# Kernel tuning notes

Hardware: AMD Instinct MI355X
Metric: run time of the kernel (lower is better)

Reference implementation:

```python
import jax, jax.numpy as jnp
import numpy as np
from jax import lax

ALPHA = 2.0       # spikingjelly ATan surrogate default alpha
NUM_HEADS = 8
V_TH = 1.0

@jax.custom_vjp
def spike(x):
    return (x >= 0.0).astype(x.dtype)

def _spike_fwd(x):
    return spike(x), x

def _spike_bwd(x, g):
    # ATan surrogate: alpha/2 / (1 + (pi/2 * alpha * x)^2)
    return (g * (ALPHA / 2.0) / (1.0 + (jnp.pi / 2.0 * ALPHA * x) ** 2),)

spike.defvjp(_spike_fwd, _spike_bwd)

def lif(x, w):
    # ParametricLIFNode, step_mode='m', decay_input=True, hard reset to 0,
    # detach_reset=True. x: [T, ...]; w: learned scalar, decay = sigmoid(w).
    decay = jax.nn.sigmoid(w)
    def step(v, xt):
        v = v + (xt - v) * decay
        s = spike(v - V_TH)
        v = v * (1.0 - lax.stop_gradient(s))  # detach_reset hard reset
        return v, s
    _, s = lax.scan(step, jnp.zeros_like(x[0]), x)
    return s

def layernorm(x, g, b, eps=1e-5):
    m = x.mean(-1, keepdims=True)
    var = ((x - m) ** 2).mean(-1, keepdims=True)
    return (x - m) / jnp.sqrt(var + eps) * g + b

def setup_inputs() -> dict:
    key = jax.random.key(0)
    ks = jax.random.split(key, 16)
    T, B, C, H, W = 4, 16, 512, 16, 16
    hidden = 4 * C
    s = 0.02
    inp = {
        'x': jax.random.normal(ks[0], (T, B, C, H, W), jnp.float32),
        'conv_w': jax.random.normal(ks[1], (C, 1, 3, 3), jnp.float32) * s,
        'conv_b': jnp.zeros((C,), jnp.float32),
        'ln1_g': jnp.ones((C,), jnp.float32),
        'ln1_b': jnp.zeros((C,), jnp.float32),
        'qkv_w': jax.random.normal(ks[2], (3 * C, C), jnp.float32) * s,
        'proj_w': jax.random.normal(ks[3], (C, C), jnp.float32) * s,
        'proj_b': jnp.zeros((C,), jnp.float32),
        'ln2_g': jnp.ones((C,), jnp.float32),
        'ln2_b': jnp.zeros((C,), jnp.float32),
        'fc1_w': jax.random.normal(ks[4], (hidden, C), jnp.float32) * s,
        'fc1_b': jnp.zeros((hidden,), jnp.float32),
        'fc2_w': jax.random.normal(ks[5], (C, hidden), jnp.float32) * s,
        'fc2_b': jnp.zeros((C,), jnp.float32),
        'lif_w': jnp.zeros((8,), jnp.float32),  # init_tau=2 -> w=0
    }
    return inp

def reference(x, conv_w, conv_b, ln1_g, ln1_b, qkv_w, proj_w, proj_b,
              ln2_g, ln2_b, fc1_w, fc1_b, fc2_w, fc2_b, lif_w):
    T, B, C, H, W = x.shape
    N = H * W
    nH = NUM_HEADS
    d = C // nH
    scale = d ** -0.5

    # conv positional embedding on spikes, residual
    s = lif(x, lif_w[0])
    sf = s.reshape(T * B, C, H, W)
    pos = lax.conv_general_dilated(
        sf, conv_w, (1, 1), 'SAME', feature_group_count=C,
        dimension_numbers=('NCHW', 'OIHW', 'NCHW'))
    pos = pos + conv_b[None, :, None, None]
    x = x + pos.reshape(T, B, C, H, W)

    # tokens: [T, B, N, C]
    xt = x.reshape(T, B, C, N).transpose(0, 1, 3, 2)

    # spiking linear attention
    h = lif(layernorm(xt, ln1_g, ln1_b), lif_w[1])
    qkv = h @ qkv_w.T                              # [T,B,N,3C]
    qkv = qkv.reshape(T, B, N, 3, nH, d).transpose(3, 0, 1, 4, 2, 5)  # [3,T,B,h,N,d]
    q = lif(qkv[0], lif_w[2])
    k = lif(qkv[1], lif_w[3])
    v = lif(qkv[2], lif_w[4])
    kv = jnp.einsum('tbhnd,tbhne->tbhde', k, v)    # [T,B,h,d,d]
    a = jnp.einsum('tbhnd,tbhde->tbhne', q, kv) * scale
    a = a.transpose(0, 1, 3, 2, 4).reshape(T, B, N, C)
    a = lif(a, lif_w[5])
    a = a @ proj_w.T + proj_b
    xt = xt + a

    # spiking MLP
    h = lif(layernorm(xt, ln2_g, ln2_b), lif_w[6])
    h = h @ fc1_w.T + fc1_b
    h = lif(h, lif_w[7])
    h = h @ fc2_w.T + fc2_b
    xt = xt + h

    return xt.transpose(0, 1, 3, 2).reshape(T, B, C, H, W)
```

## Files before the change

### kernel.cpp

```cpp
#include <hip/hip_runtime.h>

typedef unsigned long long u64;
typedef unsigned int u32;
typedef float  floatx4 __attribute__((ext_vector_type(4)));
typedef short  short8  __attribute__((ext_vector_type(8)));

#define T_ 4

static __device__ __forceinline__ float b2f(unsigned short u){
  union { unsigned int i; float f; } x; x.i = ((unsigned int)u) << 16; return x.f;
}
static __device__ __forceinline__ unsigned short f2b(float f){
  unsigned int u = __float_as_uint(f);
  unsigned int r = (u + 0x7FFFu + ((u >> 16) & 1u)) >> 16;
  return (unsigned short)r;
}
static __device__ __forceinline__ float sigmoidf_(float x){ return 1.f / (1.f + expf(-x)); }

static __device__ __forceinline__ void gll16(const void* g, void* l){
  __builtin_amdgcn_global_load_lds(
      (const __attribute__((address_space(1))) void*)g,
      (__attribute__((address_space(3))) void*)l, 16, 0, 0);
}

__global__ __launch_bounds__(256) void wsplit_kernel(const float* __restrict__ qkvw,
    const float* __restrict__ projw, const float* __restrict__ fc1w,
    const float* __restrict__ fc2w, unsigned short* __restrict__ hi,
    unsigned short* __restrict__ lo){
  int i = blockIdx.x * 256 + threadIdx.x;
  const float* src; int off;
  if (i < 786432)      { src = qkvw; off = i; }
  else if (i < 1048576){ src = projw; off = i - 786432; }
  else if (i < 2097152){ src = fc1w;  off = i - 1048576; }
  else                 { src = fc2w;  off = i - 2097152; }
  float f = src[off];
  unsigned short h = f2b(f);
  float r = f - b2f(h);
  hi[i] = h; lo[i] = f2b(r);
}

__global__ __launch_bounds__(256) void conv_lif_kernel(const float* __restrict__ x,
    const float* __restrict__ cw, const float* __restrict__ cb,
    const float* __restrict__ lifw, float* __restrict__ xt){
  __shared__ __align__(16) float xs[16 * 260];
  __shared__ u64 sbits[16][5];
  int bb = blockIdx.x & 15, cg = blockIdx.x >> 4;
  int c0 = cg * 16;
  int tid = threadIdx.x;
  int lane = tid & 63, w = tid >> 6;
  int cl = tid & 15;
  float D = sigmoidf_(lifw[0]);
  float cwv[9];
  #pragma unroll
  for (int j = 0; j < 9; ++j) cwv[j] = cw[(c0 + cl) * 9 + j];
  float cbv = cb[c0 + cl];
  float v[16];
  #pragma unroll
  for (int k = 0; k < 16; ++k) v[k] = 0.f;

  for (int t = 0; t < T_; ++t){
    #pragma unroll
    for (int j = 0; j < 4; ++j){
      int kk = __builtin_amdgcn_readfirstlane(w + 4 * j);
      const float* grow = x + (((size_t)t * 16 + bb) * 512 + c0 + kk) * 256 + lane * 4;
      gll16(grow, &xs[kk * 260]);
    }
    __syncthreads();
    #pragma unroll
    for (int k = 0; k < 16; ++k){
      float xv = xs[k * 260 + tid];
      v[k] = v[k] + (xv - v[k]) * D;
      bool sp = v[k] >= 1.f;
      u64 bal = __ballot(sp);
      if (lane == 0) sbits[k][w] = bal;
      v[k] = sp ? 0.f : v[k];
    }
    __syncthreads();
    u64 sw0 = sbits[cl][0], sw1 = sbits[cl][1], sw2 = sbits[cl][2], sw3 = sbits[cl][3];
    #pragma unroll
    for (int i = 0; i < 16; ++i){
      int n = (tid >> 4) + 16 * i;
      int hh = n >> 4, ww = n & 15;
      float acc = cbv;
      #pragma unroll
      for (int dy = -1; dy <= 1; ++dy){
        int yy = hh + dy; if ((unsigned)yy >= 16u) continue;
        #pragma unroll
        for (int dx = -1; dx <= 1; ++dx){
          int xx = ww + dx; if ((unsigned)xx >= 16u) continue;
          int p = yy * 16 + xx;
          u64 word = (p < 64) ? sw0 : (p < 128) ? sw1 : (p < 192) ? sw2 : sw3;
          if ((word >> (p & 63)) & 1ull) acc += cwv[(dy + 1) * 3 + (dx + 1)];
        }
      }
      float xv = xs[cl * 260 + n];
      xt[(((size_t)t * 16 + bb) * 256 + n) * 512 + c0 + cl] = xv + acc;
    }
    __syncthreads();
  }
}

__global__ __launch_bounds__(256) void ln_lif_kernel(const float* __restrict__ xt,
    const float* __restrict__ g, const float* __restrict__ be,
    const float* __restrict__ lifw, int lidx, u64* __restrict__ obits){
  int bn = blockIdx.x; int tid = threadIdx.x;
  int lane = tid & 63, wid = tid >> 6;
  int c0 = tid, c1 = tid + 256;
  __shared__ float ps[8];
  float D = sigmoidf_(lifw[lidx]);
  float g0 = g[c0], g1 = g[c1];
  float b0 = be[c0], b1 = be[c1];
  float v0 = 0.f, v1 = 0.f;
  for (int t = 0; t < T_; ++t){
    size_t base = ((size_t)t * 4096 + bn) * 512;
    float x0 = xt[base + c0], x1 = xt[base + c1];
    float s = x0 + x1, q = x0 * x0 + x1 * x1;
    #pragma unroll
    for (int m = 32; m > 0; m >>= 1){
      s += __shfl_xor(s, m, 64);
      q += __shfl_xor(q, m, 64);
    }
    if (lane == 0){ ps[wid * 2] = s; ps[wid * 2 + 1] = q; }
    __syncthreads();
    float S = ps[0] + ps[2] + ps[4] + ps[6];
    float Q = ps[1] + ps[3] + ps[5] + ps[7];
    __syncthreads();
    float mean = S * (1.f / 512.f);
    float var = Q * (1.f / 512.f) - mean * mean;
    float inv = 1.f / sqrtf(var + 1e-5f);
    float y0 = (x0 - mean) * inv * g0 + b0;
    float y1 = (x1 - mean) * inv * g1 + b1;
    v0 = v0 + (y0 - v0) * D; bool s0 = v0 >= 1.f;
    v1 = v1 + (y1 - v1) * D; bool s1 = v1 >= 1.f;
    u64 bal0 = __ballot(s0);
    u64 bal1 = __ballot(s1);
    if (lane == 0){
      size_t rb = ((size_t)t * 4096 + bn) * 8;
      obits[rb + wid] = bal0;
      obits[rb + 4 + wid] = bal1;
    }
    v0 = s0 ? 0.f : v0; v1 = s1 ? 0.f : v1;
  }
}

__global__ __launch_bounds__(256) void lif_bits_kernel(const float* __restrict__ in,
    u64* __restrict__ bits, const float* __restrict__ lifw, int lidx){
  int tid = blockIdx.x * 256 + threadIdx.x;
  int j = tid & 511; int bn = tid >> 9;
  float D = sigmoidf_(lifw[lidx]);
  float v = 0.f;
  #pragma unroll
  for (int t = 0; t < T_; ++t){
    int m = t * 4096 + bn;
    float xv = in[(size_t)m * 512 + j];
    v = v + (xv - v) * D;
    bool sp = v >= 1.f;
    u64 bal = __ballot(sp);
    if ((threadIdx.x & 63) == 0) bits[(size_t)m * 8 + (j >> 6)] = bal;
    v = sp ? 0.f : v;
  }
}

__global__ __launch_bounds__(256) void gemm_fused(
    const u64* __restrict__ Abits, int ars,
    const unsigned short* __restrict__ Whi, const unsigned short* __restrict__ Wlo, int ldw,
    const float* __restrict__ bias,
    float* __restrict__ xtio, float* __restrict__ outF,
    u64* __restrict__ outBits,
    int K, int mode, const float* __restrict__ lifw, int lidx){
  extern __shared__ __align__(16) char smemraw[];
  unsigned short* Bh = (unsigned short*)smemraw;
  unsigned short* Bl = (unsigned short*)(smemraw + 8192);
  u32* Alds = (u32*)(smemraw + 16384);
  u64* tab  = (u64*)(smemraw + 16384 + K * 16);
  int bn0 = blockIdx.x * 32;
  int n0  = blockIdx.y * 128;
  int tid = threadIdx.x, lane = tid & 63, wid = tid >> 6;
  int wn = wid * 32;
  int lm = lane & 15, quad = lane >> 4;
  int qs = quad * 8;
  int r4 = lane >> 2;
  int swz = ((lane & 3) ^ ((lane >> 3) & 3)) * 8;
  int rB0 = wid * 16 + r4, rB1 = rB0 + 64;
  const unsigned short* ph0 = Whi + (size_t)(n0 + rB0) * ldw + swz;
  const unsigned short* ph1 = Whi + (size_t)(n0 + rB1) * ldw + swz;
  const unsigned short* pl0 = Wlo + (size_t)(n0 + rB0) * ldw + swz;
  const unsigned short* pl1 = Wlo + (size_t)(n0 + rB1) * ldw + swz;
  int lofs = __builtin_amdgcn_readfirstlane(wid * 512);
  int sx = (quad ^ ((lm >> 1) & 3)) << 3;

  if (tid < 16){
    u64 e = 0;
    #pragma unroll
    for (int j = 0; j < 4; ++j) if ((tid >> j) & 1) e |= 0x3F80ull << (16 * j);
    tab[tid] = e;
  }
  int nw64 = K >> 6;
  for (int i = tid; i < 128 * nw64; i += 256){
    int r = i & 127, w64 = i >> 7;
    size_t g = (size_t)((r >> 5) * 4096 + bn0 + (r & 31));
    u64 vb = Abits[g * ars + w64];
    Alds[(2 * w64) * 128 + r]     = (u32)vb;
    Alds[(2 * w64 + 1) * 128 + r] = (u32)(vb >> 32);
  }

  floatx4 acc[8][2];
  #pragma unroll
  for (int i = 0; i < 8; ++i)
    #pragma unroll
    for (int j = 0; j < 2; ++j){ acc[i][j][0]=0.f; acc[i][j][1]=0.f; acc[i][j][2]=0.f; acc[i][j][3]=0.f; }

  for (int kb = 0; kb < K; kb += 32){
    gll16(ph0 + kb, Bh + lofs); gll16(ph1 + kb, Bh + 2048 + lofs);
    gll16(pl0 + kb, Bl + lofs); gll16(pl1 + kb, Bl + 2048 + lofs);
    __syncthreads();
    int wi = kb >> 5;
    short8 bh[2], bl[2];
    #pragma unroll
    for (int in = 0; in < 2; ++in){
      bh[in] = *(const short8*)(&Bh[(wn + in * 16 + lm) * 32 + sx]);
      bl[in] = *(const short8*)(&Bl[(wn + in * 16 + lm) * 32 + sx]);
    }
    #pragma unroll
    for (int im = 0; im < 8; ++im){
      u32 wv = Alds[wi * 128 + im * 16 + lm];
      u32 by = wv >> qs;
      union { u64 d[2]; short8 s; } c;
      c.d[0] = tab[by & 15u];
      c.d[1] = tab[(by >> 4) & 15u];
      acc[im][0] = __builtin_amdgcn_mfma_f32_16x16x32_bf16(c.s, bh[0], acc[im][0], 0, 0, 0);
      acc[im][1] = __builtin_amdgcn_mfma_f32_16x16x32_bf16(c.s, bh[1], acc[im][1], 0, 0, 0);
      acc[im][0] = __builtin_amdgcn_mfma_f32_16x16x32_bf16(c.s, bl[0], acc[im][0], 0, 0, 0);
      acc[im][1] = __builtin_amdgcn_mfma_f32_16x16x32_bf16(c.s, bl[1], acc[im][1], 0, 0, 0);
    }
    __syncthreads();
  }

  if (mode == 0 || mode == 3){
    #pragma unroll
    for (int im = 0; im < 8; ++im){
      int row0 = im * 16 + quad * 4;
      #pragma unroll
      for (int in = 0; in < 2; ++in){
        int col = n0 + wn + in * 16 + lm;
        float bv = bias ? bias[col] : 0.f;
        #pragma unroll
        for (int r = 0; r < 4; ++r){
          int row = row0 + r;
          int t = row >> 5; int bq = bn0 + (row & 31);
          size_t gg = (size_t)t * 4096 + bq;
          float vv = acc[im][in][r] + bv + xtio[gg * 512 + col];
          if (mode == 0){
            xtio[gg * 512 + col] = vv;
          } else {
            outF[(((size_t)t * 16 + (bq >> 8)) * 512 + col) * 256 + (bq & 255)] = vv;
          }
        }
      }
    }
    return;
  }

  u32* bits32 = (u32*)(smemraw + 20480);
  u64* ob; int obrs, obwb;
  if (mode == 1){ ob = outBits + (size_t)(n0 >> 9) * 131072; obrs = 8; obwb = (n0 & 511) >> 6; }
  else          { ob = outBits; obrs = 32; obwb = n0 >> 6; }
  float D = sigmoidf_(lifw[mode == 1 ? (2 + (n0 >> 9)) : lidx]);
  float bv0 = bias ? bias[n0 + wn + lm] : 0.f;
  float bv1 = bias ? bias[n0 + wn + 16 + lm] : 0.f;
  #pragma unroll
  for (int r = 0; r < 4; ++r){
    float vA0 = 0.f, vA1 = 0.f, vB0 = 0.f, vB1 = 0.f;
    #pragma unroll
    for (int t = 0; t < 4; ++t){
      float pA0 = acc[2*t][0][r] + bv0;   vA0 += (pA0 - vA0) * D; bool sA0 = vA0 >= 1.f; vA0 = sA0 ? 0.f : vA0;
      float pA1 = acc[2*t][1][r] + bv1;   vA1 += (pA1 - vA1) * D; bool sA1 = vA1 >= 1.f; vA1 = sA1 ? 0.f : vA1;
      float pB0 = acc[2*t+1][0][r] + bv0; vB0 += (pB0 - vB0) * D; bool sB0 = vB0 >= 1.f; vB0 = sB0 ? 0.f : vB0;
      float pB1 = acc[2*t+1][1][r] + bv1; vB1 += (pB1 - vB1) * D; bool sB1 = vB1 >= 1.f; vB1 = sB1 ? 0.f : vB1;
      u64 balA0 = __ballot(sA0), balA1 = __ballot(sA1);
      u64 balB0 = __ballot(sB0), balB1 = __ballot(sB1);
      if (lane < 4){
        int q = lane;
        u32 wA = (u32)((balA0 >> (16*q)) & 0xFFFFull) | ((u32)((balA1 >> (16*q)) & 0xFFFFull) << 16);
        u32 wB = (u32)((balB0 >> (16*q)) & 0xFFFFull) | ((u32)((balB1 >> (16*q)) & 0xFFFFull) << 16);
        bits32[(t * 32 + q * 4 + r) * 4 + wid]      = wA;
        bits32[(t * 32 + 16 + q * 4 + r) * 4 + wid] = wB;
      }
    }
  }
  __syncthreads();
  {
    int t = tid >> 6, bnl = (tid >> 1) & 31, j = tid & 1;
    size_t g = (size_t)t * 4096 + bn0 + bnl;
    int idx = (t * 32 + bnl) * 4 + 2 * j;
    u64 wv = (u64)bits32[idx] | ((u64)bits32[idx + 1] << 32);
    ob[g * obrs + obwb + j] = wv;
  }
}

__global__ __launch_bounds__(256) void attn_a_kernel(const u64* __restrict__ bits,
    float* __restrict__ aout){
  int tbh = blockIdx.x;
  int h = tbh & 7, b = (tbh >> 3) & 15, t = tbh >> 7;
  int m0 = t * 4096 + b * 256;
  int tid = threadIdx.x, lane = tid & 63, wid = tid >> 6;
  __shared__ u64 QW[256], KW[256], VW[256];
  __shared__ u64 kbt[64][4], vbt[64][4];
  __shared__ __align__(16) unsigned short Bs[64 * 72];
  {
    size_t base = (size_t)(m0 + tid) * 8 + h;
    QW[tid] = bits[base];
    KW[tid] = bits[131072 + base];
    VW[tid] = bits[262144 + base];
  }
  __syncthreads();
  {
    int i = tid & 63, w = tid >> 6;
    const u64* kwp = &KW[w * 64];
    const u64* vwp = &VW[w * 64];
    u64 bk = 0, bv = 0;
    for (int nn = 0; nn < 64; ++nn){
      bk |= ((kwp[nn] >> i) & 1ull) << nn;
      bv |= ((vwp[nn] >> i) & 1ull) << nn;
    }
    kbt[i][w] = bk; vbt[i][w] = bv;
  }
  __syncthreads();
  #pragma unroll
  for (int e = 0; e < 16; ++e){
    int idx = tid * 16 + e;
    int i = idx >> 6, j = idx & 63;
    int cnt = __popcll(kbt[i][0] & vbt[j][0]) + __popcll(kbt[i][1] & vbt[j][1])
            + __popcll(kbt[i][2] & vbt[j][2]) + __popcll(kbt[i][3] & vbt[j][3]);
    Bs[j * 72 + i] = f2b((float)cnt);
  }
  __syncthreads();
  int lm = lane & 15, quad = lane >> 4;
  int wm = wid * 64;
  u64 qw[4];
  #pragma unroll
  for (int im = 0; im < 4; ++im) qw[im] = QW[wm + im * 16 + lm];
  floatx4 acc[4][4];
  #pragma unroll
  for (int i = 0; i < 4; ++i)
    #pragma unroll
    for (int j = 0; j < 4; ++j){ acc[i][j][0]=0.f; acc[i][j][1]=0.f; acc[i][j][2]=0.f; acc[i][j][3]=0.f; }
  #pragma unroll
  for (int kb = 0; kb < 64; kb += 32){
    short8 af[4], bf[4];
    #pragma unroll
    for (int im = 0; im < 4; ++im){
      u32 byte = (u32)(qw[im] >> (kb + quad * 8)) & 0xFFu;
      union { u32 u[4]; short8 s; } c;
      c.u[0] = ((byte & 1u)        | ((byte & 2u) << 15))        * 0x3F80u;
      c.u[1] = (((byte >> 2) & 1u) | (((byte >> 3) & 1u) << 16)) * 0x3F80u;
      c.u[2] = (((byte >> 4) & 1u) | (((byte >> 5) & 1u) << 16)) * 0x3F80u;
      c.u[3] = (((byte >> 6) & 1u) | (((byte >> 7) & 1u) << 16)) * 0x3F80u;
      af[im] = c.s;
    }
    #pragma unroll
    for (int in = 0; in < 4; ++in)
      bf[in] = *(const short8*)(&Bs[(in * 16 + lm) * 72 + kb + quad * 8]);
    #pragma unroll
    for (int im = 0; im < 4; ++im)
      #pragma unroll
      for (int in = 0; in < 4; ++in)
        acc[im][in] = __builtin_amdgcn_mfma_f32_16x16x32_bf16(af[im], bf[in], acc[im][in], 0, 0, 0);
  }
  float* ob = aout + (size_t)m0 * 512 + h * 64;
  #pragma unroll
  for (int im = 0; im < 4; ++im){
    int nr0 = wm + im * 16 + quad * 4;
    #pragma unroll
    for (int in = 0; in < 4; ++in){
      int j = in * 16 + lm;
      #pragma unroll
      for (int r = 0; r < 4; ++r)
        ob[(size_t)(nr0 + r) * 512 + j] = acc[im][in][r] * 0.125f;
    }
  }
}

extern "C" void kernel_launch(void* const* d_in, const int* in_sizes, int n_in,
                              void* d_out, int out_size, void* d_ws, size_t ws_size,
                              hipStream_t stream){
  const float* x     = (const float*)d_in[0];
  const float* convw = (const float*)d_in[1];
  const float* convb = (const float*)d_in[2];
  const float* ln1g  = (const float*)d_in[3];
  const float* ln1b  = (const float*)d_in[4];
  const float* qkvw  = (const float*)d_in[5];
  const float* projw = (const float*)d_in[6];
  const float* projb = (const float*)d_in[7];
  const float* ln2g  = (const float*)d_in[8];
  const float* ln2b  = (const float*)d_in[9];
  const float* fc1w  = (const float*)d_in[10];
  const float* fc1b  = (const float*)d_in[11];
  const float* fc2w  = (const float*)d_in[12];
  const float* fc2b  = (const float*)d_in[13];
  const float* lifw  = (const float*)d_in[14];
  float* outp = (float*)d_out;

  char* wsb = (char*)d_ws;
  float* XT           = (float*)wsb;
  float* AF32         = (float*)(wsb + 33554432);
  unsigned short* WHI = (unsigned short*)(wsb + 67108864);
  unsigned short* WLO = (unsigned short*)(wsb + 73400320);
  u64* QBITS          = (u64*)(wsb + 79691776);
  u64* H12            = (u64*)(wsb + 82837504);
  u64* ASB            = (u64*)(wsb + 83886080);
  u64* HBITS          = (u64*)(wsb + 84934656);
  const int OFF_QKV = 0, OFF_PROJ = 786432, OFF_FC1 = 1048576, OFF_FC2 = 2097152;

  wsplit_kernel<<<12288, 256, 0, stream>>>(qkvw, projw, fc1w, fc2w, WHI, WLO);
  conv_lif_kernel<<<512, 256, 0, stream>>>(x, convw, convb, lifw, XT);
  ln_lif_kernel<<<4096, 256, 0, stream>>>(XT, ln1g, ln1b, lifw, 1, H12);
  gemm_fused<<<dim3(128, 12), 256, 24704, stream>>>(H12, 8,
      WHI + OFF_QKV, WLO + OFF_QKV, 512, nullptr,
      nullptr, nullptr, QBITS, 512, 1, lifw, 0);
  attn_a_kernel<<<512, 256, 0, stream>>>(QBITS, AF32);
  lif_bits_kernel<<<8192, 256, 0, stream>>>(AF32, ASB, lifw, 5);
  gemm_fused<<<dim3(128, 4), 256, 24704, stream>>>(ASB, 8,
      WHI + OFF_PROJ, WLO + OFF_PROJ, 512, projb,
      XT, nullptr, nullptr, 512, 0, lifw, 0);
  ln_lif_kernel<<<4096, 256, 0, stream>>>(XT, ln2g, ln2b, lifw, 6, H12);
  gemm_fused<<<dim3(128, 16), 256, 24704, stream>>>(H12, 8,
      WHI + OFF_FC1, WLO + OFF_FC1, 512, fc1b,
      nullptr, nullptr, HBITS, 512, 2, lifw, 7);
  gemm_fused<<<dim3(128, 4), 256, 49280, stream>>>(HBITS, 32,
      WHI + OFF_FC2, WLO + OFF_FC2, 2048, fc2b,
      XT, outp, nullptr, 2048, 3, lifw, 0);
}
```

Measured before the change: 453.0 us.

## Double-buffer weight tiles in fused GEMM and stage spike bits in chunks

After: 409.2 us. 1.11x faster.

```diff
diff --git a/kernel.cpp b/kernel.cpp
--- a/kernel.cpp
+++ b/kernel.cpp
@@ -170,9 +170,9 @@
     int K, int mode, const float* __restrict__ lifw, int lidx){
   extern __shared__ __align__(16) char smemraw[];
   unsigned short* Bh = (unsigned short*)smemraw;
-  unsigned short* Bl = (unsigned short*)(smemraw + 8192);
-  u32* Alds = (u32*)(smemraw + 16384);
-  u64* tab  = (u64*)(smemraw + 16384 + K * 16);
+  unsigned short* Bl = (unsigned short*)(smemraw + 16384);
+  u32* Alds = (u32*)(smemraw + 32768);
+  u64* tab  = (u64*)(smemraw + 40960);
   int bn0 = blockIdx.x * 32;
   int n0  = blockIdx.y * 128;
   int tid = threadIdx.x, lane = tid & 63, wid = tid >> 6;
@@ -189,20 +189,34 @@
   int lofs = __builtin_amdgcn_readfirstlane(wid * 512);
   int sx = (quad ^ ((lm >> 1) & 3)) << 3;
 
+  auto stageA = [&](int w0){
+    #pragma unroll
+    for (int i = 0; i < 4; ++i){
+      int idx = tid + i * 256;
+      int r = idx & 127, w64 = idx >> 7;
+      size_t g = (size_t)((r >> 5) * 4096 + bn0 + (r & 31));
+      u64 vb = Abits[g * ars + w0 + w64];
+      Alds[(2 * w64) * 128 + r]     = (u32)vb;
+      Alds[(2 * w64 + 1) * 128 + r] = (u32)(vb >> 32);
+    }
+  };
+  auto stageB = [&](int buf, int kb){
+    int bo = buf << 12;
+    gll16(ph0 + kb, Bh + bo + lofs);
+    gll16(ph1 + kb, Bh + bo + 2048 + lofs);
+    gll16(pl0 + kb, Bl + bo + lofs);
+    gll16(pl1 + kb, Bl + bo + 2048 + lofs);
+  };
+
   if (tid < 16){
     u64 e = 0;
     #pragma unroll
     for (int j = 0; j < 4; ++j) if ((tid >> j) & 1) e |= 0x3F80ull << (16 * j);
     tab[tid] = e;
   }
-  int nw64 = K >> 6;
-  for (int i = tid; i < 128 * nw64; i += 256){
-    int r = i & 127, w64 = i >> 7;
-    size_t g = (size_t)((r >> 5) * 4096 + bn0 + (r & 31));
-    u64 vb = Abits[g * ars + w64];
-    Alds[(2 * w64) * 128 + r]     = (u32)vb;
-    Alds[(2 * w64 + 1) * 128 + r] = (u32)(vb >> 32);
-  }
+  stageA(0);
+  stageB(0, 0);
+  __syncthreads();
 
   floatx4 acc[8][2];
   #pragma unroll
@@ -210,20 +224,25 @@
     #pragma unroll
     for (int j = 0; j < 2; ++j){ acc[i][j][0]=0.f; acc[i][j][1]=0.f; acc[i][j][2]=0.f; acc[i][j][3]=0.f; }
 
+  int cur = 0;
   for (int kb = 0; kb < K; kb += 32){
-    gll16(ph0 + kb, Bh + lofs); gll16(ph1 + kb, Bh + 2048 + lofs);
-    gll16(pl0 + kb, Bl + lofs); gll16(pl1 + kb, Bl + 2048 + lofs);
-    __syncthreads();
-    int wi = kb >> 5;
+    if (kb && (kb & 511) == 0){
+      stageA(kb >> 6);
+      __syncthreads();
+    }
+    if (kb + 32 < K) stageB(cur ^ 1, kb + 32);
+    int bo = cur << 12;
+    int wl = (kb >> 5) & 15;
     short8 bh[2], bl[2];
     #pragma unroll
     for (int in = 0; in < 2; ++in){
-      bh[in] = *(const short8*)(&Bh[(wn + in * 16 + lm) * 32 + sx]);
-      bl[in] = *(const short8*)(&Bl[(wn + in * 16 + lm) * 32 + sx]);
-    }
+      bh[in] = *(const short8*)(&Bh[bo + (wn + in * 16 + lm) * 32 + sx]);
+      bl[in] = *(const short8*)(&Bl[bo + (wn + in * 16 + lm) * 32 + sx]);
+    }
+    __builtin_amdgcn_s_setprio(1);
     #pragma unroll
     for (int im = 0; im < 8; ++im){
-      u32 wv = Alds[wi * 128 + im * 16 + lm];
+      u32 wv = Alds[wl * 128 + im * 16 + lm];
       u32 by = wv >> qs;
       union { u64 d[2]; short8 s; } c;
       c.d[0] = tab[by & 15u];
@@ -233,7 +252,9 @@
       acc[im][0] = __builtin_amdgcn_mfma_f32_16x16x32_bf16(c.s, bl[0], acc[im][0], 0, 0, 0);
       acc[im][1] = __builtin_amdgcn_mfma_f32_16x16x32_bf16(c.s, bl[1], acc[im][1], 0, 0, 0);
     }
-    __syncthreads();
+    __builtin_amdgcn_s_setprio(0);
+    __syncthreads();
+    cur ^= 1;
   }
 
   if (mode == 0 || mode == 3){
@@ -261,7 +282,7 @@
     return;
   }
 
-  u32* bits32 = (u32*)(smemraw + 20480);
+  u32* bits32 = (u32*)(smemraw + 32768);
   u64* ob; int obrs, obwb;
   if (mode == 1){ ob = outBits + (size_t)(n0 >> 9) * 131072; obrs = 8; obwb = (n0 & 511) >> 6; }
   else          { ob = outBits; obrs = 32; obwb = n0 >> 6; }
@@ -411,23 +432,24 @@
   u64* ASB            = (u64*)(wsb + 83886080);
   u64* HBITS          = (u64*)(wsb + 84934656);
   const int OFF_QKV = 0, OFF_PROJ = 786432, OFF_FC1 = 1048576, OFF_FC2 = 2097152;
+  const int GEMM_LDS = 41088;
 
   wsplit_kernel<<<12288, 256, 0, stream>>>(qkvw, projw, fc1w, fc2w, WHI, WLO);
   conv_lif_kernel<<<512, 256, 0, stream>>>(x, convw, convb, lifw, XT);
   ln_lif_kernel<<<4096, 256, 0, stream>>>(XT, ln1g, ln1b, lifw, 1, H12);
-  gemm_fused<<<dim3(128, 12), 256, 24704, stream>>>(H12, 8,
+  gemm_fused<<<dim3(128, 12), 256, GEMM_LDS, stream>>>(H12, 8,
       WHI + OFF_QKV, WLO + OFF_QKV, 512, nullptr,
       nullptr, nullptr, QBITS, 512, 1, lifw, 0);
   attn_a_kernel<<<512, 256, 0, stream>>>(QBITS, AF32);
   lif_bits_kernel<<<8192, 256, 0, stream>>>(AF32, ASB, lifw, 5);
-  gemm_fused<<<dim3(128, 4), 256, 24704, stream>>>(ASB, 8,
+  gemm_fused<<<dim3(128, 4), 256, GEMM_LDS, stream>>>(ASB, 8,
       WHI + OFF_PROJ, WLO + OFF_PROJ, 512, projb,
       XT, nullptr, nullptr, 512, 0, lifw, 0);
   ln_lif_kernel<<<4096, 256, 0, stream>>>(XT, ln2g, ln2b, lifw, 6, H12);
-  gemm_fused<<<dim3(128, 16), 256, 24704, stream>>>(H12, 8,
+  gemm_fused<<<dim3(128, 16), 256, GEMM_LDS, stream>>>(H12, 8,
       WHI + OFF_FC1, WLO + OFF_FC1, 512, fc1b,
       nullptr, nullptr, HBITS, 512, 2, lifw, 7);
-  gemm_fused<<<dim3(128, 4), 256, 49280, stream>>>(HBITS, 32,
+  gemm_fused<<<dim3(128, 4), 256, GEMM_LDS, stream>>>(HBITS, 32,
       WHI + OFF_FC2, WLO + OFF_FC2, 2048, fc2b,
       XT, outp, nullptr, 2048, 3, lifw, 0);
 }
```
